# Kernel tuning notes

Hardware: AMD Instinct MI355X
Metric: run time of the kernel (lower is better)

The kernel has to match this reference:

```python
import jax, jax.numpy as jnp
import numpy as np

N_USERS = 100000  # n_users + 1 (padding idx)
N_ITEMS = 100000  # n_items + 1
N_NODES = N_USERS + N_ITEMS
EMBED = 64
N_BEHAVIORS = 3
N_EDGES = 2000000
BATCH = 4096
REG_WEIGHT = 1e-4


def setup_inputs() -> dict:
    key = jax.random.key(0)
    ks = jax.random.split(key, 6)
    user_emb = jax.random.normal(ks[0], (N_USERS, EMBED), dtype=jnp.float32) * 0.05
    item_emb = jax.random.normal(ks[1], (N_ITEMS, EMBED), dtype=jnp.float32) * 0.05
    gcn_weight = jax.random.normal(ks[2], (N_BEHAVIORS, EMBED, EMBED), dtype=jnp.float32) * (1.0 / np.sqrt(EMBED))
    gcn_bias = jnp.zeros((N_BEHAVIORS, EMBED), dtype=jnp.float32)
    edges = jax.random.randint(ks[3], (N_BEHAVIORS, 2, N_EDGES), 0, N_NODES, dtype=jnp.int64)
    batch_data = jax.random.randint(ks[4], (BATCH, N_BEHAVIORS, 3), 0, N_USERS, dtype=jnp.int64)
    return {"user_emb": user_emb, "item_emb": item_emb, "gcn_weight": gcn_weight,
            "gcn_bias": gcn_bias, "edges": edges, "batch_data": batch_data}


def _gcn_conv(x, row, col, W, b):
    # PyG GCNConv, add_self_loops=False: out = D^-1/2 A D^-1/2 (x W) + b
    x = x @ W  # [N, d]
    deg = jax.ops.segment_sum(jnp.ones_like(col, dtype=x.dtype), col, num_segments=N_NODES)
    dinv = jnp.where(deg > 0, jax.lax.rsqrt(jnp.maximum(deg, 1.0)) * (deg > 0), 0.0)
    norm = dinv[row] * dinv[col]  # [E]
    msg = norm[:, None] * x[row]  # [E, d] gather + scale
    out = jax.ops.segment_sum(msg, col, num_segments=N_NODES)  # scatter-add
    return out + b


def _l2_normalize(x, eps=1e-12):
    n = jnp.sqrt(jnp.sum(x * x, axis=-1, keepdims=True))
    return x / jnp.maximum(n, eps)


def reference(user_emb, item_emb, gcn_weight, gcn_bias, edges, batch_data):
    total = jnp.concatenate([user_emb, item_emb], axis=0)  # [N_NODES, d]
    total_loss = jnp.float32(0.0)
    for bi in range(N_BEHAVIORS):
        row, col = edges[bi, 0], edges[bi, 1]
        layer = _gcn_conv(total, row, col, gcn_weight[bi], gcn_bias[bi])
        layer = _l2_normalize(layer)
        total = layer + total  # residual accumulation across behaviors
        u_all, i_all = total[:N_USERS], total[N_USERS:]
        users = batch_data[:, bi, 0]          # [B]
        items = batch_data[:, bi, 1:]         # [B, 2] (pos, neg)
        u_feat = u_all[users]                 # [B, d]
        i_feat = i_all[items]                 # [B, 2, d]
        scores = jnp.einsum('bd,bkd->bk', u_feat, i_feat)  # [B, 2]
        bpr = -jnp.mean(jax.nn.log_sigmoid(scores[:, 0] - scores[:, 1]))
        total_loss = total_loss + bpr
    emb_loss = 0.5 * (jnp.sum(user_emb * user_emb) + jnp.sum(item_emb * item_emb)) / BATCH
    total_loss = total_loss + REG_WEIGHT * emb_loss
    return total_loss
```

## Files before the change

### kernel.cpp

```cpp
#include <hip/hip_runtime.h>

#define N_USERS  100000
#define N_ITEMS  100000
#define N_NODES  200000
#define EMBED    64
#define NB       3
#define N_EDGESC 2000000
#define NE_TOT   (NB * N_EDGESC)
#define BATCH    4096
#define M_SEG    (NB * N_NODES)
#define NPART    500
#define PSIZE    400
#define NBUCK    (NB * NPART)
#define NBLKB    256
#define EPB      8192
#define EPB4     (EPB / 4)
#define NE4      (N_EDGESC / 4)
#define STAGE_CAP 4416
#define GEMM_BLOCKS 3125
#define AGG_BLOCKS 6250
#define BPR_BLOCKS 1024
#define NPARTS   (GEMM_BLOCKS + NB * 1024)

typedef unsigned short u16;
typedef __attribute__((ext_vector_type(8))) short short8;
typedef __attribute__((ext_vector_type(4))) float f32x4;

__device__ __forceinline__ float b2f(u16 h) {
    return __uint_as_float(((unsigned)h) << 16);
}
__device__ __forceinline__ u16 f2b(float f) {
    unsigned u = __float_as_uint(f);
    return (u16)((u + 0x7FFF + ((u >> 16) & 1)) >> 16);
}

__global__ __launch_bounds__(256) void scatterA(const int* __restrict__ edges,
                                                int* __restrict__ H) {
    __shared__ int h[NPART];
    int bi  = blockIdx.x / NBLKB;
    int blk = blockIdx.x - bi * NBLKB;
    const int4* cols4 = (const int4*)(edges + ((size_t)bi * 2 + 1) * N_EDGESC);
    for (int i = threadIdx.x; i < NPART; i += 256) h[i] = 0;
    __syncthreads();
    int b4 = blk * EPB4;
#pragma unroll 2
    for (int it = 0; it < EPB4 / 256; ++it) {
        int i4 = b4 + it * 256 + threadIdx.x;
        if (i4 < NE4) {
            int4 c = cols4[i4];
            atomicAdd(&h[c.x / PSIZE], 1);
            atomicAdd(&h[c.y / PSIZE], 1);
            atomicAdd(&h[c.z / PSIZE], 1);
            atomicAdd(&h[c.w / PSIZE], 1);
        }
    }
    __syncthreads();
    for (int i = threadIdx.x; i < NPART; i += 256)
        H[(bi * NPART + i) * NBLKB + blk] = h[i];
}

__global__ __launch_bounds__(256) void colscan(int* __restrict__ H,
                                               int* __restrict__ bCnt) {
    int wid = blockIdx.x * 4 + (threadIdx.x >> 6);
    if (wid >= NBUCK) return;
    int lane = threadIdx.x & 63;
    int carry = 0;
#pragma unroll
    for (int ch = 0; ch < NBLKB / 64; ++ch) {
        int i = wid * NBLKB + ch * 64 + lane;
        int v = H[i];
        int s = v;
#pragma unroll
        for (int off = 1; off < 64; off <<= 1) {
            int tt = __shfl_up(s, off, 64);
            if (lane >= off) s += tt;
        }
        H[i] = carry + s - v;
        carry += __shfl(s, 63, 64);
    }
    if (lane == 0) bCnt[wid] = carry;
}

__global__ __launch_bounds__(256) void scan_buckets(const int* __restrict__ bCnt,
                                                    int* __restrict__ bBase,
                                                    int* __restrict__ startv) {
    __shared__ int s[NBUCK + 1];
    __shared__ int tsum[256];
    int t = threadIdx.x;
    const int IT = (NBUCK + 255) / 256;
    int base0 = t * IT;
    int vals[IT];
    int sum = 0;
#pragma unroll
    for (int k = 0; k < IT; ++k) {
        int i = base0 + k;
        vals[k] = (i < NBUCK) ? bCnt[i] : 0;
        sum += vals[k];
    }
    tsum[t] = sum;
    __syncthreads();
    for (int off = 1; off < 256; off <<= 1) {
        int v = (t >= off) ? tsum[t - off] : 0;
        __syncthreads();
        tsum[t] += v;
        __syncthreads();
    }
    int run = tsum[t] - sum;
#pragma unroll
    for (int k = 0; k < IT; ++k) {
        int i = base0 + k;
        if (i < NBUCK) s[i] = run;
        run += vals[k];
    }
    if (t == 255) {
        s[NBUCK] = run;
        startv[M_SEG] = run;
    }
    __syncthreads();
    for (int i = t; i < NBUCK + 1; i += 256) bBase[i] = s[i];
}

__global__ __launch_bounds__(256) void scatterB(const int* __restrict__ edges,
                                                const int* __restrict__ H,
                                                const int* __restrict__ bCnt,
                                                const int* __restrict__ bBase,
                                                int* __restrict__ bpack) {
    __shared__ int cur[NPART + 2];
    __shared__ int lstart[NPART + 1];
    __shared__ int sbase[NPART];
    __shared__ int tsum[256];
    __shared__ int stage[EPB];
    int bi  = blockIdx.x / NBLKB;
    int blk = blockIdx.x - bi * NBLKB;
    const int4* rows4 = (const int4*)(edges + ((size_t)bi * 2 + 0) * N_EDGESC);
    const int4* cols4 = (const int4*)(edges + ((size_t)bi * 2 + 1) * N_EDGESC);
    int t = threadIdx.x;

    for (int i = t; i < NPART; i += 256) {
        int b  = bi * NPART + i;
        int hc = H[b * NBLKB + blk];
        int nx = (blk < NBLKB - 1) ? H[b * NBLKB + blk + 1] : bCnt[b];
        sbase[i] = bBase[b] + hc;
        cur[i]   = nx - hc;
    }
    if (t == 0) cur[NPART] = 0;
    __syncthreads();

    int sb0 = t * 2;
    int v0 = (sb0     <= NPART) ? cur[sb0]     : 0;
    int v1 = (sb0 + 1 <= NPART) ? cur[sb0 + 1] : 0;
    int sum = v0 + v1;
    tsum[t] = sum;
    __syncthreads();
    for (int off = 1; off < 256; off <<= 1) {
        int v = (t >= off) ? tsum[t - off] : 0;
        __syncthreads();
        tsum[t] += v;
        __syncthreads();
    }
    int run = tsum[t] - sum;
    __syncthreads();
    if (sb0     <= NPART) { cur[sb0]     = run;      lstart[sb0]     = run; }
    if (sb0 + 1 <= NPART) { cur[sb0 + 1] = run + v0; lstart[sb0 + 1] = run + v0; }
    __syncthreads();

    int b4 = blk * EPB4;
#pragma unroll 2
    for (int it = 0; it < EPB4 / 256; ++it) {
        int i4 = b4 + it * 256 + t;
        if (i4 < NE4) {
            int4 c = cols4[i4];
            int4 r = rows4[i4];
            { int p = c.x / PSIZE; int q = atomicAdd(&cur[p], 1);
              stage[q] = ((c.x - p * PSIZE) << 18) | r.x; }
            { int p = c.y / PSIZE; int q = atomicAdd(&cur[p], 1);
              stage[q] = ((c.y - p * PSIZE) << 18) | r.y; }
            { int p = c.z / PSIZE; int q = atomicAdd(&cur[p], 1);
              stage[q] = ((c.z - p * PSIZE) << 18) | r.z; }
            { int p = c.w / PSIZE; int q = atomicAdd(&cur[p], 1);
              stage[q] = ((c.w - p * PSIZE) << 18) | r.w; }
        }
    }
    __syncthreads();

    int grp = t >> 4;
    int li  = t & 15;
    for (int p = grp; p < NPART; p += 16) {
        int lb  = lstart[p];
        int len = lstart[p + 1] - lb;
        int gb  = sbase[p];
        for (int off = li; off < len; off += 16)
            bpack[gb + off] = stage[lb + off];
    }
}

__global__ __launch_bounds__(256) void place_kernel(const int* __restrict__ bpack,
                                                    const int* __restrict__ bBase,
                                                    int* __restrict__ startv,
                                                    float* __restrict__ dinv,
                                                    int* __restrict__ srow) {
    __shared__ int cnt[PSIZE + 2];
    __shared__ int tsum[256];
    __shared__ int stage[STAGE_CAP];
    int b    = blockIdx.x;
    int bi   = b / NPART;
    int part = b - bi * NPART;
    int segBase = bi * N_NODES + part * PSIZE;
    int lo = bBase[b], hiEnd = bBase[b + 1];
    int t = threadIdx.x;

    for (int i = t; i < PSIZE + 1; i += 256) cnt[i] = 0;
    __syncthreads();

    {
        int i = lo + t;
        for (; i + 768 < hiEnd; i += 1024) {
            int a0 = bpack[i];
            int a1 = bpack[i + 256];
            int a2 = bpack[i + 512];
            int a3 = bpack[i + 768];
            atomicAdd(&cnt[a0 >> 18], 1);
            atomicAdd(&cnt[a1 >> 18], 1);
            atomicAdd(&cnt[a2 >> 18], 1);
            atomicAdd(&cnt[a3 >> 18], 1);
        }
        for (; i < hiEnd; i += 256) atomicAdd(&cnt[bpack[i] >> 18], 1);
    }
    __syncthreads();

    int base0 = t * 2;
    int v0 = (base0     <= PSIZE) ? cnt[base0]     : 0;
    int v1 = (base0 + 1 <= PSIZE) ? cnt[base0 + 1] : 0;
    int sum = v0 + v1;
    tsum[t] = sum;
    __syncthreads();
    for (int off = 1; off < 256; off <<= 1) {
        int v = (t >= off) ? tsum[t - off] : 0;
        __syncthreads();
        tsum[t] += v;
        __syncthreads();
    }
    int run = tsum[t] - sum;
    __syncthreads();
    if (base0     <= PSIZE) cnt[base0]     = run;
    if (base0 + 1 <= PSIZE) cnt[base0 + 1] = run + v0;
    __syncthreads();

    for (int i = t; i < PSIZE; i += 256) {
        int excl = cnt[i];
        int d    = cnt[i + 1] - excl;
        startv[segBase + i] = lo + excl;
        dinv[segBase + i]   = (d > 0) ? rsqrtf((float)d) : 0.0f;
    }
    __syncthreads();

    {
        int i = lo + t;
        for (; i + 768 < hiEnd; i += 1024) {
            int p0 = bpack[i];
            int p1 = bpack[i + 256];
            int p2 = bpack[i + 512];
            int p3 = bpack[i + 768];
            int q0 = atomicAdd(&cnt[p0 >> 18], 1);
            int q1 = atomicAdd(&cnt[p1 >> 18], 1);
            int q2 = atomicAdd(&cnt[p2 >> 18], 1);
            int q3 = atomicAdd(&cnt[p3 >> 18], 1);
            if (q0 < STAGE_CAP) stage[q0] = p0 & 0x3FFFF; else srow[lo + q0] = p0 & 0x3FFFF;
            if (q1 < STAGE_CAP) stage[q1] = p1 & 0x3FFFF; else srow[lo + q1] = p1 & 0x3FFFF;
            if (q2 < STAGE_CAP) stage[q2] = p2 & 0x3FFFF; else srow[lo + q2] = p2 & 0x3FFFF;
            if (q3 < STAGE_CAP) stage[q3] = p3 & 0x3FFFF; else srow[lo + q3] = p3 & 0x3FFFF;
        }
        for (; i < hiEnd; i += 256) {
            int pk  = bpack[i];
            int pos = atomicAdd(&cnt[pk >> 18], 1);
            if (pos < STAGE_CAP) stage[pos] = pk & 0x3FFFF; else srow[lo + pos] = pk & 0x3FFFF;
        }
    }
    __syncthreads();

    int n = hiEnd - lo;
    int cap = (n < STAGE_CAP) ? n : STAGE_CAP;
    for (int i = t; i < cap; i += 256) srow[lo + i] = stage[i];
}

__device__ __forceinline__ void load_Bfrag(const float* __restrict__ W,
                                           int lane, short8 Bf[4][2]) {
    int n    = lane & 15;
    int kb   = (lane >> 4) * 8;
#pragma unroll
    for (int ct = 0; ct < 4; ++ct)
#pragma unroll
        for (int kt = 0; kt < 2; ++kt)
#pragma unroll
            for (int j = 0; j < 8; ++j)
                Bf[ct][kt][j] = (short)f2b(W[(kt * 32 + kb + j) * 64 + ct * 16 + n]);
}

__device__ __forceinline__ void store_tile(u16* __restrict__ x16,
                                           const float* __restrict__ dinv, int base,
                                           int r0, int lane, const f32x4 acc[4]) {
    int col  = lane & 15;
    int rowb = (lane >> 4) * 4;
    float dv[4];
#pragma unroll
    for (int j = 0; j < 4; ++j) dv[j] = dinv[base + r0 + rowb + j];
#pragma unroll
    for (int ct = 0; ct < 4; ++ct)
#pragma unroll
        for (int j = 0; j < 4; ++j)
            x16[(size_t)(r0 + rowb + j) * 64 + ct * 16 + col] = f2b(acc[ct][j] * dv[j]);
}

__global__ __launch_bounds__(256) void mfma_first(const float* __restrict__ ue,
                                                  const float* __restrict__ ie,
                                                  const float* __restrict__ W,
                                                  const float* __restrict__ dinv,
                                                  u16* __restrict__ x16,
                                                  float* __restrict__ regpart) {
    __shared__ float wsum[4];
    int lane = threadIdx.x & 63;
    short8 Bf[4][2];
    load_Bfrag(W, lane, Bf);

    int r0 = (blockIdx.x * 4 + (threadIdx.x >> 6)) * 16;
    int m  = lane & 15;
    int kb = (lane >> 4) * 8;
    int r  = r0 + m;
    const float* src = (r < N_USERS) ? (ue + (size_t)r * 64)
                                     : (ie + (size_t)(r - N_USERS) * 64);
    float sq = 0.0f;
    short8 A0, A1;
#pragma unroll
    for (int h = 0; h < 2; ++h) {
        float4 a = ((const float4*)(src + h * 32 + kb))[0];
        float4 b = ((const float4*)(src + h * 32 + kb))[1];
        short8& A = h ? A1 : A0;
        A[0] = (short)f2b(a.x); A[1] = (short)f2b(a.y);
        A[2] = (short)f2b(a.z); A[3] = (short)f2b(a.w);
        A[4] = (short)f2b(b.x); A[5] = (short)f2b(b.y);
        A[6] = (short)f2b(b.z); A[7] = (short)f2b(b.w);
        sq += a.x * a.x + a.y * a.y + a.z * a.z + a.w * a.w;
        sq += b.x * b.x + b.y * b.y + b.z * b.z + b.w * b.w;
    }
    f32x4 acc[4];
#pragma unroll
    for (int ct = 0; ct < 4; ++ct) {
        acc[ct] = (f32x4){0.f, 0.f, 0.f, 0.f};
        acc[ct] = __builtin_amdgcn_mfma_f32_16x16x32_bf16(A0, Bf[ct][0], acc[ct], 0, 0, 0);
        acc[ct] = __builtin_amdgcn_mfma_f32_16x16x32_bf16(A1, Bf[ct][1], acc[ct], 0, 0, 0);
    }
    store_tile(x16, dinv, 0, r0, lane, acc);

#pragma unroll
    for (int off = 32; off; off >>= 1) sq += __shfl_xor(sq, off, 64);
    if (lane == 0) wsum[threadIdx.x >> 6] = sq;
    __syncthreads();
    if (threadIdx.x == 0)
        regpart[blockIdx.x] = (wsum[0] + wsum[1] + wsum[2] + wsum[3]) *
                              (0.5f * 0.0001f / (float)BATCH);
}

__global__ __launch_bounds__(256) void gemm_bpr(const u16* __restrict__ g16,
                                                const float* __restrict__ W,
                                                const float* __restrict__ dinv,
                                                int base,
                                                u16* __restrict__ x16,
                                                const int* __restrict__ batch,
                                                int bi,
                                                float* __restrict__ bprpart) {
    __shared__ float sp4[4];
    if (blockIdx.x < GEMM_BLOCKS) {
        int lane = threadIdx.x & 63;
        short8 Bf[4][2];
        load_Bfrag(W, lane, Bf);

        int r0 = (blockIdx.x * 4 + (threadIdx.x >> 6)) * 16;
        int m  = lane & 15;
        int kb = (lane >> 4) * 8;
        const u16* src = g16 + (size_t)(r0 + m) * 64 + kb;
        short8 A0 = *(const short8*)(src);
        short8 A1 = *(const short8*)(src + 32);
        f32x4 acc[4];
#pragma unroll
        for (int ct = 0; ct < 4; ++ct) {
            acc[ct] = (f32x4){0.f, 0.f, 0.f, 0.f};
            acc[ct] = __builtin_amdgcn_mfma_f32_16x16x32_bf16(A0, Bf[ct][0], acc[ct], 0, 0, 0);
            acc[ct] = __builtin_amdgcn_mfma_f32_16x16x32_bf16(A1, Bf[ct][1], acc[ct], 0, 0, 0);
        }
        store_tile(x16, dinv, base, r0, lane, acc);
    } else {
        int blk  = blockIdx.x - GEMM_BLOCKS;
        int b    = blk * 4 + (threadIdx.x >> 6);
        int lane = threadIdx.x & 63;
        int u  = batch[((size_t)b * NB + bi) * 3 + 0];
        int i0 = batch[((size_t)b * NB + bi) * 3 + 1];
        int i1 = batch[((size_t)b * NB + bi) * 3 + 2];
        float uf = b2f(g16[(size_t)u * 64 + lane]);
        float f0 = b2f(g16[(size_t)(N_USERS + i0) * 64 + lane]);
        float f1 = b2f(g16[(size_t)(N_USERS + i1) * 64 + lane]);
        float d  = uf * (f0 - f1);
#pragma unroll
        for (int off = 32; off; off >>= 1) d += __shfl_xor(d, off, 64);
        float sp = (d > 0.0f) ? log1pf(expf(-d)) : (-d + log1pf(expf(d)));
        if (lane == 0) sp4[threadIdx.x >> 6] = sp;
        __syncthreads();
        if (threadIdx.x == 0)
            bprpart[blk] = (sp4[0] + sp4[1] + sp4[2] + sp4[3]) * (1.0f / BATCH);
    }
}

__global__ __launch_bounds__(256) void agg_kernel(const int* __restrict__ srow,
                                                  const int* __restrict__ startv,
                                                  const float* __restrict__ dinv,
                                                  const int4* __restrict__ xv,
                                                  const float4* __restrict__ reslo,
                                                  const float4* __restrict__ reshi,
                                                  const int4* __restrict__ res16,
                                                  int resf32,
                                                  int4* __restrict__ g16out,
                                                  const float* __restrict__ bias,
                                                  int base ) {
    int lane = threadIdx.x & 63;
    int li   = lane & 7;
    int c = (blockIdx.x * 4 + (threadIdx.x >> 6)) * 8 + (lane >> 3);

    int   s   = startv[base + c];
    int   end = startv[base + c + 1];
    float dc  = dinv[base + c];

    float acc[8];
#pragma unroll
    for (int d = 0; d < 8; ++d) acc[d] = 0.0f;

    int e = s;
    if (e + 8 <= end) {
        int r[8];
#pragma unroll
        for (int j = 0; j < 8; ++j) r[j] = srow[e + j];
        for (;;) {
            int  e2    = e + 8;
            bool have2 = (e2 + 8 <= end);
            int  rn[8];
            if (have2) {
#pragma unroll
                for (int j = 0; j < 8; ++j) rn[j] = srow[e2 + j];
            }
#pragma unroll
            for (int jj = 0; jj < 8; ++jj) {
                int4 w = xv[(size_t)r[jj] * 8 + li];
                acc[0] += __uint_as_float(((unsigned)w.x) << 16);
                acc[1] += __uint_as_float(((unsigned)w.x) & 0xFFFF0000u);
                acc[2] += __uint_as_float(((unsigned)w.y) << 16);
                acc[3] += __uint_as_float(((unsigned)w.y) & 0xFFFF0000u);
                acc[4] += __uint_as_float(((unsigned)w.z) << 16);
                acc[5] += __uint_as_float(((unsigned)w.z) & 0xFFFF0000u);
                acc[6] += __uint_as_float(((unsigned)w.w) << 16);
                acc[7] += __uint_as_float(((unsigned)w.w) & 0xFFFF0000u);
            }
            e = e2;
            if (!have2) break;
#pragma unroll
            for (int j = 0; j < 8; ++j) r[j] = rn[j];
        }
    }
    if (e < end) {
#pragma unroll
        for (int jj = 0; jj < 8; ++jj) {
            int  ej = e + jj;
            bool ok = ej < end;
            int  ec = ok ? ej : s;
            int  r  = srow[ec];
            int4 w  = xv[(size_t)r * 8 + li];
            float m = ok ? 1.0f : 0.0f;
            acc[0] += m * __uint_as_float(((unsigned)w.x) << 16);
            acc[1] += m * __uint_as_float(((unsigned)w.x) & 0xFFFF0000u);
            acc[2] += m * __uint_as_float(((unsigned)w.y) << 16);
            acc[3] += m * __uint_as_float(((unsigned)w.y) & 0xFFFF0000u);
            acc[4] += m * __uint_as_float(((unsigned)w.z) << 16);
            acc[5] += m * __uint_as_float(((unsigned)w.z) & 0xFFFF0000u);
            acc[6] += m * __uint_as_float(((unsigned)w.w) << 16);
            acc[7] += m * __uint_as_float(((unsigned)w.w) & 0xFFFF0000u);
        }
    }

    float4 b0 = ((const float4*)bias)[li * 2];
    float4 b1 = ((const float4*)bias)[li * 2 + 1];
    float v[8];
    v[0] = acc[0] * dc + b0.x; v[1] = acc[1] * dc + b0.y;
    v[2] = acc[2] * dc + b0.z; v[3] = acc[3] * dc + b0.w;
    v[4] = acc[4] * dc + b1.x; v[5] = acc[5] * dc + b1.y;
    v[6] = acc[6] * dc + b1.z; v[7] = acc[7] * dc + b1.w;
    float sq = 0.0f;
#pragma unroll
    for (int d = 0; d < 8; ++d) sq += v[d] * v[d];
    sq += __shfl_xor(sq, 1, 64);
    sq += __shfl_xor(sq, 2, 64);
    sq += __shfl_xor(sq, 4, 64);
    float inv = 1.0f / fmaxf(sqrtf(sq), 1e-12f);

    float rv[8];
    if (resf32) {
        const float4* rsrc = (c < N_USERS)
            ? reslo + ((size_t)c * 16 + li * 2)
            : reshi + ((size_t)(c - N_USERS) * 16 + li * 2);
        float4 t0 = rsrc[0], t1 = rsrc[1];
        rv[0] = t0.x; rv[1] = t0.y; rv[2] = t0.z; rv[3] = t0.w;
        rv[4] = t1.x; rv[5] = t1.y; rv[6] = t1.z; rv[7] = t1.w;
    } else {
        int4 rw = res16[(size_t)c * 8 + li];
        rv[0] = __uint_as_float(((unsigned)rw.x) << 16);
        rv[1] = __uint_as_float(((unsigned)rw.x) & 0xFFFF0000u);
        rv[2] = __uint_as_float(((unsigned)rw.y) << 16);
        rv[3] = __uint_as_float(((unsigned)rw.y) & 0xFFFF0000u);
        rv[4] = __uint_as_float(((unsigned)rw.z) << 16);
        rv[5] = __uint_as_float(((unsigned)rw.z) & 0xFFFF0000u);
        rv[6] = __uint_as_float(((unsigned)rw.w) << 16);
        rv[7] = __uint_as_float(((unsigned)rw.w) & 0xFFFF0000u);
    }
    float o[8];
#pragma unroll
    for (int d = 0; d < 8; ++d) o[d] = rv[d] + v[d] * inv;
    int4 h;
    h.x = (int)(((unsigned)f2b(o[0])) | (((unsigned)f2b(o[1])) << 16));
    h.y = (int)(((unsigned)f2b(o[2])) | (((unsigned)f2b(o[3])) << 16));
    h.z = (int)(((unsigned)f2b(o[4])) | (((unsigned)f2b(o[5])) << 16));
    h.w = (int)(((unsigned)f2b(o[6])) | (((unsigned)f2b(o[7])) << 16));
    g16out[(size_t)c * 8 + li] = h;
}

__global__ __launch_bounds__(256) void bpr_kernel(const u16* __restrict__ g16,
                                                  const int* __restrict__ batch,
                                                  int bi, float* __restrict__ bprpart) {
    __shared__ float sp4[4];
    int b    = blockIdx.x * 4 + (threadIdx.x >> 6);
    int lane = threadIdx.x & 63;
    int u  = batch[((size_t)b * NB + bi) * 3 + 0];
    int i0 = batch[((size_t)b * NB + bi) * 3 + 1];
    int i1 = batch[((size_t)b * NB + bi) * 3 + 2];
    float uf = b2f(g16[(size_t)u * 64 + lane]);
    float f0 = b2f(g16[(size_t)(N_USERS + i0) * 64 + lane]);
    float f1 = b2f(g16[(size_t)(N_USERS + i1) * 64 + lane]);
    float d  = uf * (f0 - f1);
#pragma unroll
    for (int off = 32; off; off >>= 1) d += __shfl_xor(d, off, 64);
    float sp = (d > 0.0f) ? log1pf(expf(-d)) : (-d + log1pf(expf(d)));
    if (lane == 0) sp4[threadIdx.x >> 6] = sp;
    __syncthreads();
    if (threadIdx.x == 0)
        bprpart[blockIdx.x] = (sp4[0] + sp4[1] + sp4[2] + sp4[3]) * (1.0f / BATCH);
}

__global__ __launch_bounds__(256) void final_write(const float* __restrict__ parts,
                                                   float* __restrict__ out) {
    __shared__ float ws[4];
    float s = 0.0f;
    for (int i = threadIdx.x; i < NPARTS; i += 256) s += parts[i];
#pragma unroll
    for (int off = 32; off; off >>= 1) s += __shfl_xor(s, off, 64);
    if ((threadIdx.x & 63) == 0) ws[threadIdx.x >> 6] = s;
    __syncthreads();
    if (threadIdx.x == 0) out[0] = ws[0] + ws[1] + ws[2] + ws[3];
}

extern "C" void kernel_launch(void* const* d_in, const int* in_sizes, int n_in,
                              void* d_out, int out_size, void* d_ws, size_t ws_size,
                              hipStream_t stream) {
    const float* user_emb = (const float*)d_in[0];
    const float* item_emb = (const float*)d_in[1];
    const float* gcn_w    = (const float*)d_in[2];
    const float* gcn_b    = (const float*)d_in[3];
    const int*   edges    = (const int*)d_in[4];
    const int*   batch    = (const int*)d_in[5];
    float*       out      = (float*)d_out;

    const size_t NODE_F = (size_t)N_NODES * EMBED;
    u16*     g16A   = (u16*)d_ws;
    u16*     g16B   = g16A + NODE_F;
    u16*     x16    = g16B + NODE_F;
    float*   dinv   = (float*)(x16 + NODE_F);
    int*     startv = (int*)(dinv + M_SEG);
    int*     Hglob  = startv + M_SEG + 1;
    int*     bCnt   = Hglob + NBUCK * NBLKB;
    int*     bBase  = bCnt + NBUCK;
    int*     bpack  = bBase + NBUCK + 1;
    int*     srow   = bpack + NE_TOT;
    float*   parts  = (float*)(srow + NE_TOT);
    float*   regpart = parts;
    float*   bprpart = parts + GEMM_BLOCKS;

    scatterA<<<NB * NBLKB, 256, 0, stream>>>(edges, Hglob);
    colscan<<<(NBUCK + 3) / 4, 256, 0, stream>>>(Hglob, bCnt);
    scan_buckets<<<1, 256, 0, stream>>>(bCnt, bBase, startv);
    scatterB<<<NB * NBLKB, 256, 0, stream>>>(edges, Hglob, bCnt, bBase, bpack);
    place_kernel<<<NBUCK, 256, 0, stream>>>(bpack, bBase, startv, dinv, srow);

    mfma_first<<<GEMM_BLOCKS, 256, 0, stream>>>(user_emb, item_emb,
                                                gcn_w, dinv, x16, regpart);

    agg_kernel<<<AGG_BLOCKS, 256, 0, stream>>>(
        srow, startv, dinv, (const int4*)x16,
        (const float4*)user_emb, (const float4*)item_emb,
        (const int4*)0, 1,
        (int4*)g16A, gcn_b, 0);

    u16* gcur = g16A;
    u16* gnxt = g16B;
    for (int bi = 1; bi < NB; ++bi) {
        gemm_bpr<<<GEMM_BLOCKS + BPR_BLOCKS, 256, 0, stream>>>(
            gcur, gcn_w + (size_t)bi * EMBED * EMBED, dinv, bi * N_NODES, x16,
            batch, bi - 1, bprpart + (size_t)(bi - 1) * BPR_BLOCKS);
        agg_kernel<<<AGG_BLOCKS, 256, 0, stream>>>(
            srow, startv, dinv, (const int4*)x16,
            (const float4*)0, (const float4*)0,
            (const int4*)gcur, 0,
            (int4*)gnxt, gcn_b + bi * EMBED, bi * N_NODES);
        u16* tmp = gcur; gcur = gnxt; gnxt = tmp;
    }
    bpr_kernel<<<BPR_BLOCKS, 256, 0, stream>>>(gcur, batch, NB - 1,
                                               bprpart + (size_t)(NB - 1) * BPR_BLOCKS);
    final_write<<<1, 256, 0, stream>>>(parts, out);
}
```

Before: 365.3 us.

## Replace two-level bucketed CSR build with direct global-atomic counting sort

Replaces the two-pass partition histogram and LDS-staged bucket scatter and placement with a simpler CSR build. It counts degrees per node using global atomics, scans per-bucket sums, writes start offsets and cursors, then scatters row indices directly through atomicAdd on per-node cursors. This removes the intermediate bpack buffer, the column scan and the in-LDS placement pass. In exchange it adds 6M contended global atomics twice and produces a nondeterministic edge order within each segment, which can hurt locality in the aggregation stage.

```diff
diff --git a/kernel.cpp b/kernel.cpp
--- a/kernel.cpp
+++ b/kernel.cpp
@@ -9,14 +9,10 @@
 #define NE_TOT   (NB * N_EDGESC)
 #define BATCH    4096
 #define M_SEG    (NB * N_NODES)
-#define NPART    500
 #define PSIZE    400
-#define NBUCK    (NB * NPART)
-#define NBLKB    256
-#define EPB      8192
-#define EPB4     (EPB / 4)
+#define NBUCK    (M_SEG / PSIZE)
 #define NE4      (N_EDGESC / 4)
-#define STAGE_CAP 4416
+#define SBLK     ((NE4 + 255) / 256)
 #define GEMM_BLOCKS 3125
 #define AGG_BLOCKS 6250
 #define BPR_BLOCKS 1024
@@ -34,51 +30,35 @@
     return (u16)((u + 0x7FFF + ((u >> 16) & 1)) >> 16);
 }
 
-__global__ __launch_bounds__(256) void scatterA(const int* __restrict__ edges,
-                                                int* __restrict__ H) {
-    __shared__ int h[NPART];
-    int bi  = blockIdx.x / NBLKB;
-    int blk = blockIdx.x - bi * NBLKB;
+__global__ __launch_bounds__(256) void degcount(const int* __restrict__ edges,
+                                                int* __restrict__ deg) {
+    int bi  = blockIdx.x / SBLK;
+    int blk = blockIdx.x - bi * SBLK;
     const int4* cols4 = (const int4*)(edges + ((size_t)bi * 2 + 1) * N_EDGESC);
-    for (int i = threadIdx.x; i < NPART; i += 256) h[i] = 0;
-    __syncthreads();
-    int b4 = blk * EPB4;
-#pragma unroll 2
-    for (int it = 0; it < EPB4 / 256; ++it) {
-        int i4 = b4 + it * 256 + threadIdx.x;
-        if (i4 < NE4) {
-            int4 c = cols4[i4];
-            atomicAdd(&h[c.x / PSIZE], 1);
-            atomicAdd(&h[c.y / PSIZE], 1);
-            atomicAdd(&h[c.z / PSIZE], 1);
-            atomicAdd(&h[c.w / PSIZE], 1);
-        }
-    }
-    __syncthreads();
-    for (int i = threadIdx.x; i < NPART; i += 256)
-        H[(bi * NPART + i) * NBLKB + blk] = h[i];
-}
-
-__global__ __launch_bounds__(256) void colscan(int* __restrict__ H,
-                                               int* __restrict__ bCnt) {
-    int wid = blockIdx.x * 4 + (threadIdx.x >> 6);
-    if (wid >= NBUCK) return;
-    int lane = threadIdx.x & 63;
-    int carry = 0;
-#pragma unroll
-    for (int ch = 0; ch < NBLKB / 64; ++ch) {
-        int i = wid * NBLKB + ch * 64 + lane;
-        int v = H[i];
-        int s = v;
-#pragma unroll
-        for (int off = 1; off < 64; off <<= 1) {
-            int tt = __shfl_up(s, off, 64);
-            if (lane >= off) s += tt;
-        }
-        H[i] = carry + s - v;
-        carry += __shfl(s, 63, 64);
-    }
-    if (lane == 0) bCnt[wid] = carry;
+    int i4 = blk * 256 + threadIdx.x;
+    if (i4 < NE4) {
+        int4 c = cols4[i4];
+        int base = bi * N_NODES;
+        atomicAdd(&deg[base + c.x], 1);
+        atomicAdd(&deg[base + c.y], 1);
+        atomicAdd(&deg[base + c.z], 1);
+        atomicAdd(&deg[base + c.w], 1);
+    }
+}
+
+__global__ __launch_bounds__(256) void bucket_sums(const int* __restrict__ deg,
+                                                   int* __restrict__ bCnt) {
+    __shared__ int ws[4];
+    int b = blockIdx.x, t = threadIdx.x;
+    int i0 = t * 2;
+    int s = 0;
+    if (i0     < PSIZE) s += deg[b * PSIZE + i0];
+    if (i0 + 1 < PSIZE) s += deg[b * PSIZE + i0 + 1];
+#pragma unroll
+    for (int off = 32; off; off >>= 1) s += __shfl_xor(s, off, 64);
+    if ((t & 63) == 0) ws[t >> 6] = s;
+    __syncthreads();
+    if (t == 0) bCnt[b] = ws[0] + ws[1] + ws[2] + ws[3];
 }
 
 __global__ __launch_bounds__(256) void scan_buckets(const int* __restrict__ bCnt,
@@ -120,35 +100,17 @@
     for (int i = t; i < NBUCK + 1; i += 256) bBase[i] = s[i];
 }
 
-__global__ __launch_bounds__(256) void scatterB(const int* __restrict__ edges,
-                                                const int* __restrict__ H,
-                                                const int* __restrict__ bCnt,
+__global__ __launch_bounds__(256) void finalize(const int* __restrict__ deg,
                                                 const int* __restrict__ bBase,
-                                                int* __restrict__ bpack) {
-    __shared__ int cur[NPART + 2];
-    __shared__ int lstart[NPART + 1];
-    __shared__ int sbase[NPART];
+                                                int* __restrict__ startv,
+                                                int* __restrict__ cursor,
+                                                float* __restrict__ dinv) {
     __shared__ int tsum[256];
-    __shared__ int stage[EPB];
-    int bi  = blockIdx.x / NBLKB;
-    int blk = blockIdx.x - bi * NBLKB;
-    const int4* rows4 = (const int4*)(edges + ((size_t)bi * 2 + 0) * N_EDGESC);
-    const int4* cols4 = (const int4*)(edges + ((size_t)bi * 2 + 1) * N_EDGESC);
-    int t = threadIdx.x;
-
-    for (int i = t; i < NPART; i += 256) {
-        int b  = bi * NPART + i;
-        int hc = H[b * NBLKB + blk];
-        int nx = (blk < NBLKB - 1) ? H[b * NBLKB + blk + 1] : bCnt[b];
-        sbase[i] = bBase[b] + hc;
-        cur[i]   = nx - hc;
-    }
-    if (t == 0) cur[NPART] = 0;
-    __syncthreads();
-
-    int sb0 = t * 2;
-    int v0 = (sb0     <= NPART) ? cur[sb0]     : 0;
-    int v1 = (sb0 + 1 <= NPART) ? cur[sb0 + 1] : 0;
+    int b = blockIdx.x, t = threadIdx.x;
+    int base = b * PSIZE;
+    int i0 = t * 2;
+    int v0 = (i0     < PSIZE) ? deg[base + i0]     : 0;
+    int v1 = (i0 + 1 < PSIZE) ? deg[base + i0 + 1] : 0;
     int sum = v0 + v1;
     tsum[t] = sum;
     __syncthreads();
@@ -159,128 +121,42 @@
         __syncthreads();
     }
     int run = tsum[t] - sum;
-    __syncthreads();
-    if (sb0     <= NPART) { cur[sb0]     = run;      lstart[sb0]     = run; }
-    if (sb0 + 1 <= NPART) { cur[sb0 + 1] = run + v0; lstart[sb0 + 1] = run + v0; }
-    __syncthreads();
-
-    int b4 = blk * EPB4;
-#pragma unroll 2
-    for (int it = 0; it < EPB4 / 256; ++it) {
-        int i4 = b4 + it * 256 + t;
-        if (i4 < NE4) {
-            int4 c = cols4[i4];
-            int4 r = rows4[i4];
-            { int p = c.x / PSIZE; int q = atomicAdd(&cur[p], 1);
-              stage[q] = ((c.x - p * PSIZE) << 18) | r.x; }
-            { int p = c.y / PSIZE; int q = atomicAdd(&cur[p], 1);
-              stage[q] = ((c.y - p * PSIZE) << 18) | r.y; }
-            { int p = c.z / PSIZE; int q = atomicAdd(&cur[p], 1);
-              stage[q] = ((c.z - p * PSIZE) << 18) | r.z; }
-            { int p = c.w / PSIZE; int q = atomicAdd(&cur[p], 1);
-              stage[q] = ((c.w - p * PSIZE) << 18) | r.w; }
-        }
-    }
-    __syncthreads();
-
-    int grp = t >> 4;
-    int li  = t & 15;
-    for (int p = grp; p < NPART; p += 16) {
-        int lb  = lstart[p];
-        int len = lstart[p + 1] - lb;
-        int gb  = sbase[p];
-        for (int off = li; off < len; off += 16)
-            bpack[gb + off] = stage[lb + off];
-    }
-}
-
-__global__ __launch_bounds__(256) void place_kernel(const int* __restrict__ bpack,
-                                                    const int* __restrict__ bBase,
-                                                    int* __restrict__ startv,
-                                                    float* __restrict__ dinv,
-                                                    int* __restrict__ srow) {
-    __shared__ int cnt[PSIZE + 2];
-    __shared__ int tsum[256];
-    __shared__ int stage[STAGE_CAP];
-    int b    = blockIdx.x;
-    int bi   = b / NPART;
-    int part = b - bi * NPART;
-    int segBase = bi * N_NODES + part * PSIZE;
-    int lo = bBase[b], hiEnd = bBase[b + 1];
-    int t = threadIdx.x;
-
-    for (int i = t; i < PSIZE + 1; i += 256) cnt[i] = 0;
-    __syncthreads();
-
-    {
-        int i = lo + t;
-        for (; i + 768 < hiEnd; i += 1024) {
-            int a0 = bpack[i];
-            int a1 = bpack[i + 256];
-            int a2 = bpack[i + 512];
-            int a3 = bpack[i + 768];
-            atomicAdd(&cnt[a0 >> 18], 1);
-            atomicAdd(&cnt[a1 >> 18], 1);
-            atomicAdd(&cnt[a2 >> 18], 1);
-            atomicAdd(&cnt[a3 >> 18], 1);
-        }
-        for (; i < hiEnd; i += 256) atomicAdd(&cnt[bpack[i] >> 18], 1);
-    }
-    __syncthreads();
-
-    int base0 = t * 2;
-    int v0 = (base0     <= PSIZE) ? cnt[base0]     : 0;
-    int v1 = (base0 + 1 <= PSIZE) ? cnt[base0 + 1] : 0;
-    int sum = v0 + v1;
-    tsum[t] = sum;
-    __syncthreads();
-    for (int off = 1; off < 256; off <<= 1) {
-        int v = (t >= off) ? tsum[t - off] : 0;
-        __syncthreads();
-        tsum[t] += v;
-        __syncthreads();
-    }
-    int run = tsum[t] - sum;
-    __syncthreads();
-    if (base0     <= PSIZE) cnt[base0]     = run;
-    if (base0 + 1 <= PSIZE) cnt[base0 + 1] = run + v0;
-    __syncthreads();
-
-    for (int i = t; i < PSIZE; i += 256) {
-        int excl = cnt[i];
-        int d    = cnt[i + 1] - excl;
-        startv[segBase + i] = lo + excl;
-        dinv[segBase + i]   = (d > 0) ? rsqrtf((float)d) : 0.0f;
-    }
-    __syncthreads();
-
-    {
-        int i = lo + t;
-        for (; i + 768 < hiEnd; i += 1024) {
-            int p0 = bpack[i];
-            int p1 = bpack[i + 256];
-            int p2 = bpack[i + 512];
-            int p3 = bpack[i + 768];
-            int q0 = atomicAdd(&cnt[p0 >> 18], 1);
-            int q1 = atomicAdd(&cnt[p1 >> 18], 1);
-            int q2 = atomicAdd(&cnt[p2 >> 18], 1);
-            int q3 = atomicAdd(&cnt[p3 >> 18], 1);
-            if (q0 < STAGE_CAP) stage[q0] = p0 & 0x3FFFF; else srow[lo + q0] = p0 & 0x3FFFF;
-            if (q1 < STAGE_CAP) stage[q1] = p1 & 0x3FFFF; else srow[lo + q1] = p1 & 0x3FFFF;
-            if (q2 < STAGE_CAP) stage[q2] = p2 & 0x3FFFF; else srow[lo + q2] = p2 & 0x3FFFF;
-            if (q3 < STAGE_CAP) stage[q3] = p3 & 0x3FFFF; else srow[lo + q3] = p3 & 0x3FFFF;
-        }
-        for (; i < hiEnd; i += 256) {
-            int pk  = bpack[i];
-            int pos = atomicAdd(&cnt[pk >> 18], 1);
-            if (pos < STAGE_CAP) stage[pos] = pk & 0x3FFFF; else srow[lo + pos] = pk & 0x3FFFF;
-        }
-    }
-    __syncthreads();
-
-    int n = hiEnd - lo;
-    int cap = (n < STAGE_CAP) ? n : STAGE_CAP;
-    for (int i = t; i < cap; i += 256) srow[lo + i] = stage[i];
+    int gb  = bBase[b];
+    if (i0 < PSIZE) {
+        int sv = gb + run;
+        startv[base + i0] = sv;
+        cursor[base + i0] = sv;
+        dinv[base + i0]   = (v0 > 0) ? rsqrtf((float)v0) : 0.0f;
+    }
+    if (i0 + 1 < PSIZE) {
+        int sv = gb + run + v0;
+        startv[base + i0 + 1] = sv;
+        cursor[base + i0 + 1] = sv;
+        dinv[base + i0 + 1]   = (v1 > 0) ? rsqrtf((float)v1) : 0.0f;
+    }
+}
+
+__global__ __launch_bounds__(256) void scatter_direct(const int* __restrict__ edges,
+                                                      int* __restrict__ cursor,
+                                                      int* __restrict__ srow) {
+    int bi  = blockIdx.x / SBLK;
+    int blk = blockIdx.x - bi * SBLK;
+    const int4* rows4 = (const int4*)(edges + ((size_t)bi * 2 + 0) * N_EDGESC);
+    const int4* cols4 = (const int4*)(edges + ((size_t)bi * 2 + 1) * N_EDGESC);
+    int i4 = blk * 256 + threadIdx.x;
+    if (i4 < NE4) {
+        int4 c = cols4[i4];
+        int4 r = rows4[i4];
+        int base = bi * N_NODES;
+        int p0 = atomicAdd(&cursor[base + c.x], 1);
+        int p1 = atomicAdd(&cursor[base + c.y], 1);
+        int p2 = atomicAdd(&cursor[base + c.z], 1);
+        int p3 = atomicAdd(&cursor[base + c.w], 1);
+        srow[p0] = r.x;
+        srow[p1] = r.y;
+        srow[p2] = r.z;
+        srow[p3] = r.w;
+    }
 }
 
 __device__ __forceinline__ void load_Bfrag(const float* __restrict__ W,
@@ -579,20 +455,21 @@
     u16*     x16    = g16B + NODE_F;
     float*   dinv   = (float*)(x16 + NODE_F);
     int*     startv = (int*)(dinv + M_SEG);
-    int*     Hglob  = startv + M_SEG + 1;
-    int*     bCnt   = Hglob + NBUCK * NBLKB;
+    int*     deg    = startv + M_SEG + 1;
+    int*     cursor = deg + M_SEG;
+    int*     bCnt   = cursor + M_SEG;
     int*     bBase  = bCnt + NBUCK;
-    int*     bpack  = bBase + NBUCK + 1;
-    int*     srow   = bpack + NE_TOT;
+    int*     srow   = bBase + NBUCK + 1;
     float*   parts  = (float*)(srow + NE_TOT);
     float*   regpart = parts;
     float*   bprpart = parts + GEMM_BLOCKS;
 
-    scatterA<<<NB * NBLKB, 256, 0, stream>>>(edges, Hglob);
-    colscan<<<(NBUCK + 3) / 4, 256, 0, stream>>>(Hglob, bCnt);
+    hipMemsetAsync(deg, 0, (size_t)M_SEG * sizeof(int), stream);
+    degcount<<<NB * SBLK, 256, 0, stream>>>(edges, deg);
+    bucket_sums<<<NBUCK, 256, 0, stream>>>(deg, bCnt);
     scan_buckets<<<1, 256, 0, stream>>>(bCnt, bBase, startv);
-    scatterB<<<NB * NBLKB, 256, 0, stream>>>(edges, Hglob, bCnt, bBase, bpack);
-    place_kernel<<<NBUCK, 256, 0, stream>>>(bpack, bBase, startv, dinv, srow);
+    finalize<<<NBUCK, 256, 0, stream>>>(deg, bBase, startv, cursor, dinv);
+    scatter_direct<<<NB * SBLK, 256, 0, stream>>>(edges, cursor, srow);
 
     mfma_first<<<GEMM_BLOCKS, 256, 0, stream>>>(user_emb, item_emb,
                                                 gcn_w, dinv, x16, regpart);
```

Result: slower. 1.087 ms (+197.7%).
